# Performance work log

Hardware: AMD Instinct MI355X
Metric: run time of the kernel (lower is better)

The kernel has to match this reference:

```python
import jax, jax.numpy as jnp
import numpy as np

VOCAB = 32000
EMBED = 1024
BATCH = 16384
SEQ = 7


def _convolute(X, kernel):
    # X: (B, L, E); kernel: (h, E) -> (B, L-h+1, E)
    h = kernel.shape[0]
    L = X.shape[1]
    out = X[:, 0:L - h + 1] * kernel[0]
    for t in range(1, h):
        out = out + X[:, t:L - h + 1 + t] * kernel[t]
    return out


def setup_inputs() -> dict:
    key = jax.random.key(0)
    k1, k2, k3, k4, k5, k6 = jax.random.split(key, 6)
    X = jax.random.randint(k1, (BATCH, SEQ), 0, VOCAB)
    emb = jax.random.normal(k2, (VOCAB, EMBED), dtype=jnp.float32)
    conv1 = jax.random.normal(k3, (2, EMBED), dtype=jnp.float32)
    conv2 = jax.random.normal(k4, (2, EMBED), dtype=jnp.float32)
    conv3 = jax.random.normal(k5, (3, EMBED), dtype=jnp.float32)
    conv4 = jax.random.normal(k6, (3, EMBED), dtype=jnp.float32)
    return {"X": X, "emb": emb, "conv1": conv1, "conv2": conv2,
            "conv3": conv3, "conv4": conv4}


def reference(X, emb, conv1, conv2, conv3, conv4):
    H = emb[X]                                  # (B, 7, E)
    H = jax.nn.sigmoid(_convolute(H, conv1))    # (B, 6, E)
    H = jax.nn.sigmoid(_convolute(H, conv2))    # (B, 5, E)
    H = jax.nn.sigmoid(_convolute(H, conv3))    # (B, 3, E)
    H = jax.nn.sigmoid(_convolute(H, conv4))    # (B, 1, E)  (scentence_size == 7)
    return H.reshape(H.shape[0], -1)            # (B, E)
```

## Files before the change

### kernel.cpp

```cpp
#include <hip/hip_runtime.h>
#include <hip/hip_bf16.h>


constexpr int EMBED = 1024;
constexpr int SEQ   = 7;

typedef float f2 __attribute__((ext_vector_type(2)));

__device__ __forceinline__ f2 sig2(f2 y) {
    f2 u;
    u.x = __builtin_amdgcn_exp2f(y.x);
    u.y = __builtin_amdgcn_exp2f(y.y);
    f2 d = u + (f2){1.0f, 1.0f};
    f2 r;
    r.x = __builtin_amdgcn_rcpf(d.x);
    r.y = __builtin_amdgcn_rcpf(d.y);
    return r;
}

__global__ __launch_bounds__(256) void CSM_62216896250023_kernel(
    const int*   __restrict__ X,
    const float* __restrict__ emb,
    const float* __restrict__ c1,
    const float* __restrict__ c2,
    const float* __restrict__ c3,
    const float* __restrict__ c4,
    float*       __restrict__ out)
{
    const int b = blockIdx.x;
    const int e = threadIdx.x << 2;

    int idx[SEQ];
#pragma unroll
    for (int t = 0; t < SEQ; ++t) idx[t] = X[b * SEQ + t];

    f2 v[SEQ][2];
#pragma unroll
    for (int t = 0; t < SEQ; ++t) {
        const float4 f = *(const float4*)(emb + (size_t)idx[t] * EMBED + e);
        v[t][0] = (f2){f.x, f.y};
        v[t][1] = (f2){f.z, f.w};
    }

    const float NL2E = -1.44269504088896f;
    f2 k1[2][2], k2[2][2], k3[3][2], k4[3][2];
#pragma unroll
    for (int t = 0; t < 2; ++t) {
        float4 f = *(const float4*)(c1 + t * EMBED + e);
        k1[t][0] = (f2){f.x * NL2E, f.y * NL2E};
        k1[t][1] = (f2){f.z * NL2E, f.w * NL2E};
        f = *(const float4*)(c2 + t * EMBED + e);
        k2[t][0] = (f2){f.x * NL2E, f.y * NL2E};
        k2[t][1] = (f2){f.z * NL2E, f.w * NL2E};
    }
#pragma unroll
    for (int t = 0; t < 3; ++t) {
        float4 f = *(const float4*)(c3 + t * EMBED + e);
        k3[t][0] = (f2){f.x * NL2E, f.y * NL2E};
        k3[t][1] = (f2){f.z * NL2E, f.w * NL2E};
        f = *(const float4*)(c4 + t * EMBED + e);
        k4[t][0] = (f2){f.x * NL2E, f.y * NL2E};
        k4[t][1] = (f2){f.z * NL2E, f.w * NL2E};
    }

    f2 o[2];
#pragma unroll
    for (int p = 0; p < 2; ++p) {
        f2 h1[6];
#pragma unroll
        for (int l = 0; l < 6; ++l)
            h1[l] = sig2(v[l][p] * k1[0][p] + v[l + 1][p] * k1[1][p]);

        f2 h2[5];
#pragma unroll
        for (int l = 0; l < 5; ++l)
            h2[l] = sig2(h1[l] * k2[0][p] + h1[l + 1] * k2[1][p]);

        f2 h3[3];
#pragma unroll
        for (int l = 0; l < 3; ++l)
            h3[l] = sig2(h2[l] * k3[0][p] + h2[l + 1] * k3[1][p] + h2[l + 2] * k3[2][p]);

        o[p] = sig2(h3[0] * k4[0][p] + h3[1] * k4[1][p] + h3[2] * k4[2][p]);
    }

    float4 of;
    of.x = o[0].x; of.y = o[0].y; of.z = o[1].x; of.w = o[1].y;
    *(float4*)(out + (size_t)b * EMBED + e) = of;
}

extern "C" void kernel_launch(void* const* d_in, const int* in_sizes, int n_in,
                              void* d_out, int out_size, void* d_ws, size_t ws_size,
                              hipStream_t stream) {
    const int*   X   = (const int*)d_in[0];
    const float* emb = (const float*)d_in[1];
    const float* c1  = (const float*)d_in[2];
    const float* c2  = (const float*)d_in[3];
    const float* c3  = (const float*)d_in[4];
    const float* c4  = (const float*)d_in[5];
    float* out = (float*)d_out;

    const int batch = in_sizes[0] / SEQ;
    CSM_62216896250023_kernel<<<batch, 256, 0, stream>>>(X, emb, c1, c2, c3, c4, out);
}
```

Before: 256.1 us.

## Process eight rows per block with double-buffered embedding gathers

Each block now handles eight batch rows instead of one. Conv weights are loaded once per block and reused across those rows. Embedding gathers for the next row are issued before the current row is computed, using two register buffers to overlap memory latency with the sigmoid math. This cuts the grid size by a factor of eight and raises register pressure, with launch bounds asking for four blocks per CU. The launch assumes the batch divides evenly by eight.

```diff
diff --git a/kernel.cpp b/kernel.cpp
--- a/kernel.cpp
+++ b/kernel.cpp
@@ -1,9 +1,9 @@
 #include <hip/hip_runtime.h>
-#include <hip/hip_bf16.h>
 
 
 constexpr int EMBED = 1024;
 constexpr int SEQ   = 7;
+constexpr int ROWS  = 8;
 
 typedef float f2 __attribute__((ext_vector_type(2)));
 
@@ -18,7 +18,47 @@
     return r;
 }
 
-__global__ __launch_bounds__(256) void CSM_62216896250023_kernel(
+struct Weights {
+    f2 k1[2][2], k2[2][2], k3[3][2], k4[3][2];
+};
+
+__device__ __forceinline__ void gather_row(const float* __restrict__ emb,
+                                           const int* __restrict__ X,
+                                           int row, int e, f2 v[SEQ][2]) {
+#pragma unroll
+    for (int t = 0; t < SEQ; ++t) {
+        const int id = X[row * SEQ + t];
+        const float4 f = *(const float4*)(emb + (size_t)id * EMBED + e);
+        v[t][0] = (f2){f.x, f.y};
+        v[t][1] = (f2){f.z, f.w};
+    }
+}
+
+__device__ __forceinline__ void compute_row(const f2 v[SEQ][2], const Weights& w,
+                                            float* __restrict__ outp) {
+    f2 o[2];
+#pragma unroll
+    for (int p = 0; p < 2; ++p) {
+        f2 h1[6];
+#pragma unroll
+        for (int l = 0; l < 6; ++l)
+            h1[l] = sig2(v[l][p] * w.k1[0][p] + v[l + 1][p] * w.k1[1][p]);
+        f2 h2[5];
+#pragma unroll
+        for (int l = 0; l < 5; ++l)
+            h2[l] = sig2(h1[l] * w.k2[0][p] + h1[l + 1] * w.k2[1][p]);
+        f2 h3[3];
+#pragma unroll
+        for (int l = 0; l < 3; ++l)
+            h3[l] = sig2(h2[l] * w.k3[0][p] + h2[l + 1] * w.k3[1][p] + h2[l + 2] * w.k3[2][p]);
+        o[p] = sig2(h3[0] * w.k4[0][p] + h3[1] * w.k4[1][p] + h3[2] * w.k4[2][p]);
+    }
+    float4 of;
+    of.x = o[0].x; of.y = o[0].y; of.z = o[1].x; of.w = o[1].y;
+    *(float4*)outp = of;
+}
+
+__global__ __launch_bounds__(256, 4) void CSM_62216896250023_kernel(
     const int*   __restrict__ X,
     const float* __restrict__ emb,
     const float* __restrict__ c1,
@@ -27,66 +67,42 @@
     const float* __restrict__ c4,
     float*       __restrict__ out)
 {
-    const int b = blockIdx.x;
-    const int e = threadIdx.x << 2;
-
-    int idx[SEQ];
-#pragma unroll
-    for (int t = 0; t < SEQ; ++t) idx[t] = X[b * SEQ + t];
-
-    f2 v[SEQ][2];
-#pragma unroll
-    for (int t = 0; t < SEQ; ++t) {
-        const float4 f = *(const float4*)(emb + (size_t)idx[t] * EMBED + e);
-        v[t][0] = (f2){f.x, f.y};
-        v[t][1] = (f2){f.z, f.w};
-    }
+    const int b0 = blockIdx.x * ROWS;
+    const int e  = threadIdx.x << 2;
 
     const float NL2E = -1.44269504088896f;
-    f2 k1[2][2], k2[2][2], k3[3][2], k4[3][2];
+    Weights w;
 #pragma unroll
     for (int t = 0; t < 2; ++t) {
         float4 f = *(const float4*)(c1 + t * EMBED + e);
-        k1[t][0] = (f2){f.x * NL2E, f.y * NL2E};
-        k1[t][1] = (f2){f.z * NL2E, f.w * NL2E};
+        w.k1[t][0] = (f2){f.x * NL2E, f.y * NL2E};
+        w.k1[t][1] = (f2){f.z * NL2E, f.w * NL2E};
         f = *(const float4*)(c2 + t * EMBED + e);
-        k2[t][0] = (f2){f.x * NL2E, f.y * NL2E};
-        k2[t][1] = (f2){f.z * NL2E, f.w * NL2E};
+        w.k2[t][0] = (f2){f.x * NL2E, f.y * NL2E};
+        w.k2[t][1] = (f2){f.z * NL2E, f.w * NL2E};
     }
 #pragma unroll
     for (int t = 0; t < 3; ++t) {
         float4 f = *(const float4*)(c3 + t * EMBED + e);
-        k3[t][0] = (f2){f.x * NL2E, f.y * NL2E};
-        k3[t][1] = (f2){f.z * NL2E, f.w * NL2E};
+        w.k3[t][0] = (f2){f.x * NL2E, f.y * NL2E};
+        w.k3[t][1] = (f2){f.z * NL2E, f.w * NL2E};
         f = *(const float4*)(c4 + t * EMBED + e);
-        k4[t][0] = (f2){f.x * NL2E, f.y * NL2E};
-        k4[t][1] = (f2){f.z * NL2E, f.w * NL2E};
+        w.k4[t][0] = (f2){f.x * NL2E, f.y * NL2E};
+        w.k4[t][1] = (f2){f.z * NL2E, f.w * NL2E};
     }
 
-    f2 o[2];
+    f2 va[SEQ][2], vb[SEQ][2];
+    gather_row(emb, X, b0, e, va);
 #pragma unroll
-    for (int p = 0; p < 2; ++p) {
-        f2 h1[6];
-#pragma unroll
-        for (int l = 0; l < 6; ++l)
-            h1[l] = sig2(v[l][p] * k1[0][p] + v[l + 1][p] * k1[1][p]);
-
-        f2 h2[5];
-#pragma unroll
-        for (int l = 0; l < 5; ++l)
-            h2[l] = sig2(h1[l] * k2[0][p] + h1[l + 1] * k2[1][p]);
-
-        f2 h3[3];
-#pragma unroll
-        for (int l = 0; l < 3; ++l)
-            h3[l] = sig2(h2[l] * k3[0][p] + h2[l + 1] * k3[1][p] + h2[l + 2] * k3[2][p]);
-
-        o[p] = sig2(h3[0] * k4[0][p] + h3[1] * k4[1][p] + h3[2] * k4[2][p]);
+    for (int r = 0; r < ROWS; ++r) {
+        if (r & 1) {
+            if (r + 1 < ROWS) gather_row(emb, X, b0 + r + 1, e, va);
+            compute_row(vb, w, out + (size_t)(b0 + r) * EMBED + e);
+        } else {
+            if (r + 1 < ROWS) gather_row(emb, X, b0 + r + 1, e, vb);
+            compute_row(va, w, out + (size_t)(b0 + r) * EMBED + e);
+        }
     }
-
-    float4 of;
-    of.x = o[0].x; of.y = o[0].y; of.z = o[1].x; of.w = o[1].y;
-    *(float4*)(out + (size_t)b * EMBED + e) = of;
 }
 
 extern "C" void kernel_launch(void* const* d_in, const int* in_sizes, int n_in,
@@ -101,5 +117,5 @@
     float* out = (float*)d_out;
 
     const int batch = in_sizes[0] / SEQ;
-    CSM_62216896250023_kernel<<<batch, 256, 0, stream>>>(X, emb, c1, c2, c3, c4, out);
+    CSM_62216896250023_kernel<<<batch / ROWS, 256, 0, stream>>>(X, emb, c1, c2, c3, c4, out);
 }
```

Result: faster. 246.9 us (-3.6%).
